# Optimization experiments

Measured on AMD Instinct MI355X. Metric: run time of the kernel, lower is better.

## Reference

```python
import jax, jax.numpy as jnp
import numpy as np

N_BLOCK = 3
N_NODES = 20000
N_EDGES = 320000
N_GRAPHS = 200
F = 128          # n_hidden_feat = n_GCN_feat
FE = 3 * F       # concat [ni, nj, delta]
K1 = 36          # N_shbf * N_srbf
K2 = 26          # plane-wave feature dim (hard-coded in source)


def setup_inputs() -> dict:
    key = jax.random.key(0)
    ks = jax.random.split(key, 20)
    s = 0.05
    inp = {
        "nodes": jax.random.normal(ks[0], (N_NODES, F), jnp.float32),
        "edge_sources": jax.random.randint(ks[1], (N_EDGES,), 0, N_NODES),
        "edge_targets": jax.random.randint(ks[2], (N_EDGES,), 0, N_NODES),
        # keep distances away from 0 to avoid blowing up (nj-ni)/rij
        "edge_distance": jax.random.uniform(ks[3], (N_EDGES,), jnp.float32, 0.5, 1.5),
        "graph_indices": jax.random.randint(ks[4], (N_NODES,), 0, N_GRAPHS),
        "node_counts": jnp.ones((N_GRAPHS,), jnp.float32) * (N_NODES / N_GRAPHS),
        "combine_sets": jax.random.normal(ks[5], (N_EDGES, K1), jnp.float32),
        "plane_wave": jax.random.normal(ks[6], (N_EDGES, K2), jnp.float32),
        # parameters ([in, out] layout; torch Linear has bias=False here)
        "W_emb": jax.random.normal(ks[7], (F, F), jnp.float32) * s,
        "Wg": jax.random.normal(ks[8], (N_BLOCK, FE, F), jnp.float32) * s,
        "Wm": jax.random.normal(ks[9], (N_BLOCK, FE, F), jnp.float32) * s,
        "W1v": jax.random.normal(ks[10], (N_BLOCK, K1, F), jnp.float32) * s,
        "W2v": jax.random.normal(ks[11], (N_BLOCK, K2, F), jnp.float32) * s,
        "W2vg": jax.random.normal(ks[12], (N_BLOCK, K2, F), jnp.float32) * s,
        "Wp1": jax.random.normal(ks[13], (N_BLOCK, F, F), jnp.float32) * s,
        "Wp2": jax.random.normal(ks[14], (N_BLOCK, F, F), jnp.float32) * s,
        "Wpsi": jax.random.normal(ks[15], (N_BLOCK, F, F), jnp.float32) * s,
        "Wlr1": jax.random.normal(ks[16], (F, F // 2), jnp.float32) * s,
        "Wlr2": jax.random.normal(ks[17], (F // 2, F // 3), jnp.float32) * s,
        "Wlr3": jax.random.normal(ks[18], (F // 3, 1), jnp.float32) * s,
    }
    return inp


def reference(nodes, edge_sources, edge_targets, edge_distance, graph_indices,
              node_counts, combine_sets, plane_wave,
              W_emb, Wg, Wm, W1v, W2v, W2vg, Wp1, Wp2, Wpsi, Wlr1, Wlr2, Wlr3):
    G = node_counts.shape[0]
    # NodeEmbedding: Linear + Sigmoid
    x = jax.nn.sigmoid(nodes @ W_emb)
    pools = []
    for i in range(N_BLOCK):
        # GatedGraphConvolution: edge gather -> concat -> gated MLP -> scatter-add
        ni = x[edge_sources]                      # [E, F]
        nj = x[edge_targets]                      # [E, F]
        delta = (nj - ni) / edge_distance[:, None]
        fe = jnp.concatenate([ni, nj, delta], axis=1)   # [E, 3F]
        e_gate = jax.nn.sigmoid(fe @ Wg[i])
        e_mlp = jax.nn.elu(fe @ Wm[i])
        z1 = combine_sets @ W1v[i]                # note: linear1_vector_gate unused in source forward
        z2 = (plane_wave @ W2v[i]) * jax.nn.sigmoid(plane_wave @ W2vg[i])
        z = e_gate * e_mlp * (z1 + z2)            # [E, F]
        x = x.at[edge_sources].add(z)             # output = input.clone(); index_add_
        # Gated_pooling (division by node_counts is discarded in the source -> plain segment sum)
        zp = jax.nn.elu(x @ Wp1[i])
        pools.append(jax.ops.segment_sum(zp * (x @ Wp2[i]), graph_indices, num_segments=G))
        # MLP_psi2n
        x = jax.nn.elu(x @ Wpsi[i])
    out = pools[0] + pools[1] + pools[2]          # sum over blocks, [G, F]
    out = jax.nn.elu(out @ Wlr1)
    out = jax.nn.elu(out @ Wlr2)
    out = out @ Wlr3                              # [G, 1]
    return out.squeeze()
```

## Files before the change

### kernel.cpp

```cpp
#include <hip/hip_runtime.h>
#include <math.h>

#define NNODES 20000
#define NEDGES 320000
#define NGRAPHS 200
#define K1 36
#define K2 26

struct WPtrs { const float* w[6]; };

__device__ __forceinline__ float sigf(float v) { return 1.0f / (1.0f + expf(-v)); }
__device__ __forceinline__ float eluf(float v) { return v > 0.0f ? v : expm1f(v); }

__global__ __launch_bounds__(256) void gemm128_kernel(
    const float* __restrict__ A, WPtrs wp, float* __restrict__ out,
    int out_stride, int act)
{
    __shared__ float4 Wl[2048];
    __shared__ float4 Al[2048];

    const int half  = blockIdx.y & 1;
    const int chunk = blockIdx.y >> 1;
    const float4* W4 = (const float4*)(wp.w[chunk] + half * 64);

    for (int idx = threadIdx.x; idx < 2048; idx += 256) {
        int k = idx >> 4, fq = idx & 15;
        Wl[idx] = W4[k * 32 + fq];
    }
    const int m0 = blockIdx.x * 64;
    const float4* A4 = (const float4*)A;
    for (int idx = threadIdx.x; idx < 2048; idx += 256) {
        int r = idx >> 5, k4 = idx & 31;
        int row = m0 + r;
        Al[idx] = (row < NNODES) ? A4[(size_t)row * 32 + k4] : make_float4(0.f, 0.f, 0.f, 0.f);
    }
    __syncthreads();

    const int fg = threadIdx.x & 15;
    const int ng = threadIdx.x >> 4;

    float acc[4][4] = {};
    #pragma unroll 4
    for (int k4 = 0; k4 < 32; ++k4) {
        float4 a[4], w[4];
        #pragma unroll
        for (int j = 0; j < 4; ++j) a[j] = Al[(ng * 4 + j) * 32 + k4];
        #pragma unroll
        for (int q = 0; q < 4; ++q) w[q] = Wl[(k4 * 4 + q) * 16 + fg];
        #pragma unroll
        for (int j = 0; j < 4; ++j) {
            const float* ap = (const float*)&a[j];
            #pragma unroll
            for (int q = 0; q < 4; ++q) {
                const float* wq = (const float*)&w[q];
                #pragma unroll
                for (int jj = 0; jj < 4; ++jj)
                    acc[j][jj] = fmaf(ap[q], wq[jj], acc[j][jj]);
            }
        }
    }

    const int coff = chunk * 128 + half * 64 + fg * 4;
    #pragma unroll
    for (int j = 0; j < 4; ++j) {
        int row = m0 + ng * 4 + j;
        if (row < NNODES) {
            float4 v; float* vp = (float*)&v;
            #pragma unroll
            for (int jj = 0; jj < 4; ++jj) {
                float t = acc[j][jj];
                vp[jj] = act ? sigf(t) : t;
            }
            *(float4*)(out + (size_t)row * out_stride + coff) = v;
        }
    }
}

__global__ __launch_bounds__(256) void edge_kernel(
    const float* __restrict__ P,
    const int* __restrict__ esrc, const int* __restrict__ etgt,
    const float* __restrict__ dist,
    const float* __restrict__ cs, const float* __restrict__ pw,
    const float* __restrict__ W1v, const float* __restrict__ W2v,
    const float* __restrict__ W2vg,
    float* __restrict__ x)
{
    const int f    = threadIdx.x & 127;
    const int esub = threadIdx.x >> 7;

    float w1[K1], w2[K2], w2g[K2];
    #pragma unroll
    for (int k = 0; k < K1; ++k) w1[k]  = W1v[k * 128 + f];
    #pragma unroll
    for (int k = 0; k < K2; ++k) w2[k]  = W2v[k * 128 + f];
    #pragma unroll
    for (int k = 0; k < K2; ++k) w2g[k] = W2vg[k * 128 + f];

    const int ebase = blockIdx.x * 64 + esub;
    for (int it = 0; it < 32; ++it) {
        const int e = __builtin_amdgcn_readfirstlane(ebase + it * 2);
        const int s = esrc[e];
        const int t = etgt[e];
        const float invd = 1.0f / dist[e];

        const float* csr = cs + (size_t)e * K1;
        const float* pwr = pw + (size_t)e * K2;
        float z1 = 0.f, za = 0.f, zb = 0.f;
        #pragma unroll
        for (int k = 0; k < K1; ++k) z1 = fmaf(csr[k], w1[k], z1);
        #pragma unroll
        for (int k = 0; k < K2; ++k) {
            float p = pwr[k];
            za = fmaf(p, w2[k],  za);
            zb = fmaf(p, w2g[k], zb);
        }

        const float* Ps = P + (size_t)s * 768;
        const float* Pt = P + (size_t)t * 768;
        float g = Ps[f]       + Pt[128 + f] + (Pt[256 + f] - Ps[256 + f]) * invd;
        float m = Ps[384 + f] + Pt[512 + f] + (Pt[640 + f] - Ps[640 + f]) * invd;

        float z = sigf(g) * eluf(m) * (z1 + za * sigf(zb));
        atomicAdd(x + (size_t)s * 128 + f, z);
    }
}

__global__ __launch_bounds__(256) void pool_psi_kernel(
    const float* __restrict__ T, const int* __restrict__ gidx,
    float* __restrict__ pools, float* __restrict__ xout)
{
    int idx = blockIdx.x * 256 + threadIdx.x;
    int n = idx >> 7, f = idx & 127;
    float h1 = eluf(T[(size_t)n * 384 + f]);
    float h2 = T[(size_t)n * 384 + 128 + f];
    atomicAdd(pools + (size_t)gidx[n] * 128 + f, h1 * h2);
    xout[(size_t)n * 128 + f] = eluf(T[(size_t)n * 384 + 256 + f]);
}

__global__ __launch_bounds__(64) void final_kernel(
    const float* __restrict__ pools,
    const float* __restrict__ Wlr1, const float* __restrict__ Wlr2,
    const float* __restrict__ Wlr3, float* __restrict__ out)
{
    __shared__ float h1[64];
    __shared__ float h2[42];
    const int g = blockIdx.x;
    const int f = threadIdx.x;

    float a = 0.f;
    #pragma unroll 8
    for (int k = 0; k < 128; ++k) a = fmaf(pools[(size_t)g * 128 + k], Wlr1[k * 64 + f], a);
    h1[f] = eluf(a);
    __syncthreads();
    if (f < 42) {
        float b = 0.f;
        #pragma unroll
        for (int k = 0; k < 64; ++k) b = fmaf(h1[k], Wlr2[k * 42 + f], b);
        h2[f] = eluf(b);
    }
    __syncthreads();
    if (f == 0) {
        float c = 0.f;
        #pragma unroll
        for (int k = 0; k < 42; ++k) c = fmaf(h2[k], Wlr3[k], c);
        out[g] = c;
    }
}

__global__ void zero_kernel(float* p, int n)
{
    int i = blockIdx.x * 256 + threadIdx.x;
    if (i < n) p[i] = 0.f;
}

extern "C" void kernel_launch(void* const* d_in, const int* in_sizes, int n_in,
                              void* d_out, int out_size, void* d_ws, size_t ws_size,
                              hipStream_t stream)
{
    const float* nodes = (const float*)d_in[0];
    const int*   esrc  = (const int*)d_in[1];
    const int*   etgt  = (const int*)d_in[2];
    const float* dist  = (const float*)d_in[3];
    const int*   gidx  = (const int*)d_in[4];
    const float* cs    = (const float*)d_in[6];
    const float* pw    = (const float*)d_in[7];
    const float* W_emb = (const float*)d_in[8];
    const float* Wg    = (const float*)d_in[9];
    const float* Wm    = (const float*)d_in[10];
    const float* W1v   = (const float*)d_in[11];
    const float* W2v   = (const float*)d_in[12];
    const float* W2vg  = (const float*)d_in[13];
    const float* Wp1   = (const float*)d_in[14];
    const float* Wp2   = (const float*)d_in[15];
    const float* Wpsi  = (const float*)d_in[16];
    const float* Wlr1  = (const float*)d_in[17];
    const float* Wlr2  = (const float*)d_in[18];
    const float* Wlr3  = (const float*)d_in[19];
    float* outp = (float*)d_out;

    float* xA    = (float*)d_ws;
    float* xB    = xA + (size_t)NNODES * 128;
    float* P     = xB + (size_t)NNODES * 128;
    float* pools = P + (size_t)NNODES * 768;

    zero_kernel<<<100, 256, 0, stream>>>(pools, NGRAPHS * 128);

    {
        WPtrs wp{}; wp.w[0] = W_emb;
        gemm128_kernel<<<dim3(313, 2), 256, 0, stream>>>(nodes, wp, xA, 128, 1);
    }

    float* xc = xA;
    float* xn = xB;
    for (int i = 0; i < 3; ++i) {
        WPtrs wp{};
        const float* Wgi = Wg + (size_t)i * 49152;
        const float* Wmi = Wm + (size_t)i * 49152;
        wp.w[0] = Wgi;          wp.w[1] = Wgi + 16384;  wp.w[2] = Wgi + 32768;
        wp.w[3] = Wmi;          wp.w[4] = Wmi + 16384;  wp.w[5] = Wmi + 32768;
        gemm128_kernel<<<dim3(313, 12), 256, 0, stream>>>(xc, wp, P, 768, 0);

        edge_kernel<<<5000, 256, 0, stream>>>(P, esrc, etgt, dist, cs, pw,
            W1v + (size_t)i * (K1 * 128),
            W2v + (size_t)i * (K2 * 128),
            W2vg + (size_t)i * (K2 * 128), xc);

        WPtrs wq{};
        wq.w[0] = Wp1 + (size_t)i * 16384;
        wq.w[1] = Wp2 + (size_t)i * 16384;
        wq.w[2] = Wpsi + (size_t)i * 16384;
        gemm128_kernel<<<dim3(313, 6), 256, 0, stream>>>(xc, wq, P, 384, 0);

        pool_psi_kernel<<<10000, 256, 0, stream>>>(P, gidx, pools, xn);

        float* tmp = xc; xc = xn; xn = tmp;
    }

    final_kernel<<<NGRAPHS, 64, 0, stream>>>(pools, Wlr1, Wlr2, Wlr3, outp);
}
```

Measured before the change: 1.332 ms.

## Batch four edges per wave in edge kernel with weights staged in LDS

The edge kernel now moves the W1v/W2v/W2vg weights from per-thread registers into a padded LDS tile read as float4. Each wave handles four edges per iteration, loading all gathered P rows up front to raise memory-level parallelism and sharing each weight read across four edges. Blocks cover 128 edges each, and waves-per-EU is pinned to 3 to bound register use. The cost is extra LDS traffic, fewer blocks in flight, and higher register pressure from the four-edge batch.

```diff
diff --git a/kernel.cpp b/kernel.cpp
--- a/kernel.cpp
+++ b/kernel.cpp
@@ -6,6 +6,8 @@
 #define NGRAPHS 200
 #define K1 36
 #define K2 26
+#define EPB 128
+#define WPITCH 92
 
 struct WPtrs { const float* w[6]; };
 
@@ -76,7 +78,9 @@
     }
 }
 
-__global__ __launch_bounds__(256) void edge_kernel(
+__global__ __launch_bounds__(256)
+__attribute__((amdgpu_waves_per_eu(3, 3)))
+void edge_kernel(
     const float* __restrict__ P,
     const int* __restrict__ esrc, const int* __restrict__ etgt,
     const float* __restrict__ dist,
@@ -85,43 +89,107 @@
     const float* __restrict__ W2vg,
     float* __restrict__ x)
 {
-    const int f    = threadIdx.x & 127;
-    const int esub = threadIdx.x >> 7;
-
-    float w1[K1], w2[K2], w2g[K2];
-    #pragma unroll
-    for (int k = 0; k < K1; ++k) w1[k]  = W1v[k * 128 + f];
-    #pragma unroll
-    for (int k = 0; k < K2; ++k) w2[k]  = W2v[k * 128 + f];
-    #pragma unroll
-    for (int k = 0; k < K2; ++k) w2g[k] = W2vg[k * 128 + f];
-
-    const int ebase = blockIdx.x * 64 + esub;
-    for (int it = 0; it < 32; ++it) {
-        const int e = __builtin_amdgcn_readfirstlane(ebase + it * 2);
-        const int s = esrc[e];
-        const int t = etgt[e];
-        const float invd = 1.0f / dist[e];
-
-        const float* csr = cs + (size_t)e * K1;
-        const float* pwr = pw + (size_t)e * K2;
-        float z1 = 0.f, za = 0.f, zb = 0.f;
-        #pragma unroll
-        for (int k = 0; k < K1; ++k) z1 = fmaf(csr[k], w1[k], z1);
-        #pragma unroll
-        for (int k = 0; k < K2; ++k) {
-            float p = pwr[k];
-            za = fmaf(p, w2[k],  za);
-            zb = fmaf(p, w2g[k], zb);
-        }
-
-        const float* Ps = P + (size_t)s * 768;
-        const float* Pt = P + (size_t)t * 768;
-        float g = Ps[f]       + Pt[128 + f] + (Pt[256 + f] - Ps[256 + f]) * invd;
-        float m = Ps[384 + f] + Pt[512 + f] + (Pt[640 + f] - Ps[640 + f]) * invd;
-
-        float z = sigf(g) * eluf(m) * (z1 + za * sigf(zb));
-        atomicAdd(x + (size_t)s * 128 + f, z);
+    __shared__ float Wt[128 * WPITCH];
+
+    const int tid  = threadIdx.x;
+    const int f    = tid & 127;
+    const int esub = tid >> 7;
+
+    for (int kk = esub; kk < WPITCH; kk += 2) {
+        float v = 0.f;
+        if (kk < 36)                   v = W1v[kk * 128 + f];
+        else if (kk < 62)              v = W2v[(kk - 36) * 128 + f];
+        else if (kk >= 64 && kk < 90)  v = W2vg[(kk - 64) * 128 + f];
+        Wt[f * WPITCH + kk] = v;
+    }
+    __syncthreads();
+
+    const float* Wrow = &Wt[f * WPITCH];
+    const int ebase = blockIdx.x * EPB + esub * 4;
+
+    for (int g = 0; g < EPB / 8; ++g) {
+        const int e0 = __builtin_amdgcn_readfirstlane(ebase + g * 8);
+
+        int sA[4], tA[4]; float dA[4];
+        #pragma unroll
+        for (int j = 0; j < 4; ++j) {
+            sA[j] = esrc[e0 + j];
+            tA[j] = etgt[e0 + j];
+            dA[j] = dist[e0 + j];
+        }
+
+        float gv[4][8];
+        #pragma unroll
+        for (int j = 0; j < 4; ++j) {
+            const float* Ps = P + (size_t)sA[j] * 768;
+            const float* Pt = P + (size_t)tA[j] * 768;
+            gv[j][0] = Ps[f];        gv[j][1] = Pt[128 + f];
+            gv[j][2] = Pt[256 + f];  gv[j][3] = Ps[256 + f];
+            gv[j][4] = Ps[384 + f];  gv[j][5] = Pt[512 + f];
+            gv[j][6] = Pt[640 + f];  gv[j][7] = Ps[640 + f];
+        }
+
+        float z1[4] = {0.f, 0.f, 0.f, 0.f};
+        float za[4] = {0.f, 0.f, 0.f, 0.f};
+        float zb[4] = {0.f, 0.f, 0.f, 0.f};
+
+        const float* cp0 = cs + (size_t)(e0 + 0) * K1;
+        const float* cp1 = cs + (size_t)(e0 + 1) * K1;
+        const float* cp2 = cs + (size_t)(e0 + 2) * K1;
+        const float* cp3 = cs + (size_t)(e0 + 3) * K1;
+        #pragma unroll
+        for (int c = 0; c < 9; ++c) {
+            float4 w = *(const float4*)(Wrow + c * 4);
+            const float* wq = (const float*)&w;
+            #pragma unroll
+            for (int q = 0; q < 4; ++q) {
+                z1[0] = fmaf(cp0[c * 4 + q], wq[q], z1[0]);
+                z1[1] = fmaf(cp1[c * 4 + q], wq[q], z1[1]);
+                z1[2] = fmaf(cp2[c * 4 + q], wq[q], z1[2]);
+                z1[3] = fmaf(cp3[c * 4 + q], wq[q], z1[3]);
+            }
+        }
+
+        const float* qp0 = pw + (size_t)(e0 + 0) * K2;
+        const float* qp1 = pw + (size_t)(e0 + 1) * K2;
+        const float* qp2 = pw + (size_t)(e0 + 2) * K2;
+        const float* qp3 = pw + (size_t)(e0 + 3) * K2;
+        #pragma unroll
+        for (int c = 0; c < 6; ++c) {
+            float4 w2 = *(const float4*)(Wrow + 36 + c * 4);
+            float4 wg = *(const float4*)(Wrow + 64 + c * 4);
+            const float* w2q = (const float*)&w2;
+            const float* wgq = (const float*)&wg;
+            #pragma unroll
+            for (int q = 0; q < 4; ++q) {
+                float p0 = qp0[c * 4 + q], p1 = qp1[c * 4 + q];
+                float p2 = qp2[c * 4 + q], p3 = qp3[c * 4 + q];
+                za[0] = fmaf(p0, w2q[q], za[0]);  zb[0] = fmaf(p0, wgq[q], zb[0]);
+                za[1] = fmaf(p1, w2q[q], za[1]);  zb[1] = fmaf(p1, wgq[q], zb[1]);
+                za[2] = fmaf(p2, w2q[q], za[2]);  zb[2] = fmaf(p2, wgq[q], zb[2]);
+                za[3] = fmaf(p3, w2q[q], za[3]);  zb[3] = fmaf(p3, wgq[q], zb[3]);
+            }
+        }
+        {
+            float2 w2t = *(const float2*)(Wrow + 60);
+            float2 wgt = *(const float2*)(Wrow + 88);
+            #pragma unroll
+            for (int j = 0; j < 4; ++j) {
+                const float* qpj = (j == 0) ? qp0 : (j == 1) ? qp1 : (j == 2) ? qp2 : qp3;
+                float p24 = qpj[24], p25 = qpj[25];
+                za[j] = fmaf(p24, w2t.x, fmaf(p25, w2t.y, za[j]));
+                zb[j] = fmaf(p24, wgt.x, fmaf(p25, wgt.y, zb[j]));
+            }
+        }
+
+        #pragma unroll
+        for (int j = 0; j < 4; ++j) {
+            float invd = 1.0f / dA[j];
+            float gsum = gv[j][0] + gv[j][1] + (gv[j][2] - gv[j][3]) * invd;
+            float msum = gv[j][4] + gv[j][5] + (gv[j][6] - gv[j][7]) * invd;
+            float z = sigf(gsum) * eluf(msum) * (z1[j] + za[j] * sigf(zb[j]));
+            atomicAdd(x + (size_t)sA[j] * 128 + f, z);
+        }
     }
 }
 
@@ -220,7 +288,7 @@
         wp.w[3] = Wmi;          wp.w[4] = Wmi + 16384;  wp.w[5] = Wmi + 32768;
         gemm128_kernel<<<dim3(313, 12), 256, 0, stream>>>(xc, wp, P, 768, 0);
 
-        edge_kernel<<<5000, 256, 0, stream>>>(P, esrc, etgt, dist, cs, pw,
+        edge_kernel<<<NEDGES / EPB, 256, 0, stream>>>(P, esrc, etgt, dist, cs, pw,
             W1v + (size_t)i * (K1 * 128),
             W2v + (size_t)i * (K2 * 128),
             W2vg + (size_t)i * (K2 * 128), xc);
```

Result: slower. 1.731 ms (+30.0%).
